# Kernel tuning notes

Hardware: AMD Instinct MI355X
Metric: run time of the kernel (lower is better)

## Reference

```python
import jax, jax.numpy as jnp
import numpy as np

B, K, D = 8, 4000, 256
H, DQ, DV = 8, 32, 32
WIN, PAD = 200, 50
STEP = WIN - 2 * PAD  # 100
BETA = 0.25


def setup_inputs() -> dict:
    key = jax.random.key(0)
    ks = jax.random.split(key, 14)
    s = 0.02
    return {
        "query": jax.random.normal(ks[0], (B, K, D), jnp.float32),
        "key": jax.random.normal(ks[1], (B, K, D), jnp.float32),
        "value": jax.random.normal(ks[2], (B, K, D), jnp.float32),
        "Wq": jax.random.normal(ks[3], (D, H * DQ), jnp.float32) * s,
        "bq": jax.random.normal(ks[4], (H * DQ,), jnp.float32) * s,
        "Wk": jax.random.normal(ks[5], (D, H * DQ), jnp.float32) * s,
        "bk": jax.random.normal(ks[6], (H * DQ,), jnp.float32) * s,
        "Wv": jax.random.normal(ks[7], (D, H * DV), jnp.float32) * s,
        "bv": jax.random.normal(ks[8], (H * DV,), jnp.float32) * s,
        "Wo": jax.random.normal(ks[9], (H * DV, D), jnp.float32) * s,
        "bo": jax.random.normal(ks[10], (D,), jnp.float32) * s,
    }


def _windows(x, n_win):
    starts = jnp.arange(n_win) * STEP
    idx = starts[:, None] + jnp.arange(WIN)[None, :]
    return x[:, :, idx, :]


def reference(query, key, value, Wq, bq, Wk, bk, Wv, bv, Wo, bo):
    b, k_len, d = query.shape
    pad = lambda t: jnp.pad(t, ((0, 0), (PAD, PAD), (0, 0)), mode='edge')  # replicate pad
    qp, kp, vp = pad(query), pad(key), pad(value)
    kpad = k_len + 2 * PAD
    n_win = (kpad - WIN) // STEP + 1

    def proj(x, Wm, bias, dh):
        y = x @ Wm + bias                       # [B, Kp, H*dh]
        return y.reshape(b, kpad, H, dh).transpose(0, 2, 1, 3)  # [B, H, Kp, dh]

    q = _windows(proj(qp, Wq, bq, DQ), n_win)
    kk = _windows(proj(kp, Wk, bk, DQ), n_win)
    v = _windows(proj(vp, Wv, bv, DV), n_win)

    scores = jnp.einsum('bhnid,bhnjd->bhnij', q, kk) / jnp.sqrt(jnp.float32(WIN))
    dist = jnp.abs(jnp.arange(WIN)[:, None] - jnp.arange(WIN)[None, :]).astype(scores.dtype)
    cauchy = (1.0 / (1.0 + BETA * dist * dist)) * (1.0 - jnp.eye(WIN, dtype=scores.dtype))
    scores = scores * cauchy
    causal = jnp.triu(jnp.ones((WIN, WIN), dtype=bool), k=1)  # attention_size is not None -> causal masking
    scores = jnp.where(causal, -jnp.inf, scores)
    attn = jax.nn.softmax(scores, axis=-1)
    out = jnp.einsum('bhnij,bhnjd->bhnid', attn, v)
    out = out[:, :, :, PAD:WIN - PAD, :].reshape(b, H, k_len, DV)
    out = out.transpose(0, 2, 1, 3).reshape(b, k_len, H * DV)  # heads concatenated, head-major slices
    return out @ Wo + bo
```

## Files before the change

kernel.cpp:

```cpp
#include <hip/hip_runtime.h>


typedef __bf16 bf16_t;
typedef __bf16 bf16x8 __attribute__((ext_vector_type(8)));
typedef float  f32x4  __attribute__((ext_vector_type(4)));

#define MFMA16(a, b, c) __builtin_amdgcn_mfma_f32_16x16x32_bf16((a), (b), (c), 0, 0, 0)

static __device__ __forceinline__ bf16x8 cvt8(float4 a, float4 b) {
  bf16x8 r;
  r[0] = (bf16_t)a.x; r[1] = (bf16_t)a.y; r[2] = (bf16_t)a.z; r[3] = (bf16_t)a.w;
  r[4] = (bf16_t)b.x; r[5] = (bf16_t)b.y; r[6] = (bf16_t)b.z; r[7] = (bf16_t)b.w;
  return r;
}

static __device__ __forceinline__ unsigned short bbits(bf16_t v) {
  union { bf16_t b; unsigned short u; } c; c.b = v; return c.u;
}

__global__ __launch_bounds__(256)
void prep_weights(const float* __restrict__ Wq, const float* __restrict__ Wk,
                  const float* __restrict__ Wv, const float* __restrict__ Wo,
                  bf16_t* __restrict__ wt) {
  const int mat  = blockIdx.x >> 6;
  const int tile = blockIdx.x & 63;
  const int kt = (tile >> 3) * 32, nt = (tile & 7) * 32;
  const float* W = (mat == 0) ? Wq : (mat == 1) ? Wk : (mat == 2) ? Wv : Wo;
  __shared__ float t[32][33];
  const int tx = threadIdx.x & 31, ty = threadIdx.x >> 5;
#pragma unroll
  for (int i = 0; i < 32; i += 8)
    t[ty + i][tx] = W[(size_t)(kt + ty + i) * 256 + nt + tx];
  __syncthreads();
  bf16_t* dst = wt + (size_t)mat * 65536;
#pragma unroll
  for (int i = 0; i < 32; i += 8)
    dst[(size_t)(nt + ty + i) * 256 + kt + tx] = (bf16_t)t[tx][ty + i];
}

template <int MODE>
__global__ __launch_bounds__(256)
void gemm256(const void* __restrict__ Xv, const bf16_t* __restrict__ Wt,
             const float* __restrict__ bias, void* __restrict__ Out, int M) {
  constexpr bool INB = (MODE == 3);
  const int m0 = blockIdx.x * 128;
  const int n0 = blockIdx.y * 128;
  __shared__ bf16_t la[128 * 40];
  __shared__ bf16_t lb[128 * 40];
  const int tid  = threadIdx.x;
  const int lane = tid & 63;
  const int wr   = ((tid >> 7) & 1) * 64;
  const int wc   = ((tid >> 6) & 1) * 64;
  const int lo   = lane & 15, hi = lane >> 4;
  const int arow = tid >> 1;
  const int acol = (tid & 1) * 16;
  int ar = m0 + arow; if (ar >= M) ar = M - 1;

  f32x4 acc[4][4] = {};

  for (int kk = 0; kk < 256; kk += 32) {
    if constexpr (!INB) {
      const float* X = (const float*)Xv + (size_t)ar * 256 + kk + acol;
      float4 x0 = ((const float4*)X)[0];
      float4 x1 = ((const float4*)X)[1];
      float4 x2 = ((const float4*)X)[2];
      float4 x3 = ((const float4*)X)[3];
      *(bf16x8*)&la[arow * 40 + acol]     = cvt8(x0, x1);
      *(bf16x8*)&la[arow * 40 + acol + 8] = cvt8(x2, x3);
    } else {
      const bf16_t* X = (const bf16_t*)Xv + (size_t)ar * 256 + kk + acol;
      *(bf16x8*)&la[arow * 40 + acol]     = ((const bf16x8*)X)[0];
      *(bf16x8*)&la[arow * 40 + acol + 8] = ((const bf16x8*)X)[1];
    }
    {
      const bf16_t* Wp = Wt + (size_t)(n0 + arow) * 256 + kk + acol;
      *(bf16x8*)&lb[arow * 40 + acol]     = ((const bf16x8*)Wp)[0];
      *(bf16x8*)&lb[arow * 40 + acol + 8] = ((const bf16x8*)Wp)[1];
    }
    __syncthreads();

    bf16x8 af[4], bfv[4];
#pragma unroll
    for (int mi = 0; mi < 4; ++mi)
      af[mi] = *(const bf16x8*)&la[(wr + mi * 16 + lo) * 40 + hi * 8];
#pragma unroll
    for (int ni = 0; ni < 4; ++ni)
      bfv[ni] = *(const bf16x8*)&lb[(wc + ni * 16 + lo) * 40 + hi * 8];
#pragma unroll
    for (int mi = 0; mi < 4; ++mi)
#pragma unroll
      for (int ni = 0; ni < 4; ++ni)
        acc[mi][ni] = MFMA16(af[mi], bfv[ni], acc[mi][ni]);
    __syncthreads();
  }

#pragma unroll
  for (int mi = 0; mi < 4; ++mi)
#pragma unroll
    for (int ni = 0; ni < 4; ++ni) {
      const int n   = n0 + wc + ni * 16 + lo;
      const float bia = bias[n];
      const int mb  = m0 + wr + mi * 16 + hi * 4;
      if (mb >= M) continue;
      if constexpr (MODE == 0) {
        bf16_t* O = (bf16_t*)Out;
#pragma unroll
        for (int r = 0; r < 4; ++r)
          O[(size_t)(mb + r) * 256 + n] = (bf16_t)(acc[mi][ni][r] + bia);
      } else if constexpr (MODE == 1) {
        const int b = mb / 4000, t = mb - b * 4000;
        bf16_t* O = (bf16_t*)Out;
#pragma unroll
        for (int r = 0; r < 4; ++r)
          O[((size_t)b * 4064 + t + 50 + r) * 256 + n] = (bf16_t)(acc[mi][ni][r] + bia);
      } else if constexpr (MODE == 2) {
        const int b = mb / 4000, t = mb - b * 4000;
        const int h = n >> 5, dv = n & 31;
        bf16_t* O = (bf16_t*)Out + ((size_t)((b * 8 + h) * 32 + dv)) * 4064 + t + 50;
        unsigned short e0 = bbits((bf16_t)(acc[mi][ni][0] + bia));
        unsigned short e1 = bbits((bf16_t)(acc[mi][ni][1] + bia));
        unsigned short e2 = bbits((bf16_t)(acc[mi][ni][2] + bia));
        unsigned short e3 = bbits((bf16_t)(acc[mi][ni][3] + bia));
        unsigned* O32 = (unsigned*)O;
        O32[0] = (unsigned)e0 | ((unsigned)e1 << 16);
        O32[1] = (unsigned)e2 | ((unsigned)e3 << 16);
      } else {
        float* O = (float*)Out;
#pragma unroll
        for (int r = 0; r < 4; ++r)
          O[(size_t)(mb + r) * 256 + n] = acc[mi][ni][r] + bia;
      }
    }
}

__global__ void fill_edges(bf16_t* __restrict__ kb, bf16_t* __restrict__ vt, int nb) {
  const int idx = blockIdx.x * 256 + threadIdx.x;
  const int kcnt = nb * 64 * 256;
  if (idx < kcnt) {
    const int b  = idx >> 14;
    const int pp = (idx >> 8) & 63;
    const int nn = idx & 255;
    const int p  = (pp < 50) ? pp : pp + 4000;
    bf16_t v = (pp < 50) ? kb[((size_t)b * 4064 + 50) * 256 + nn] : (bf16_t)0.f;
    kb[((size_t)b * 4064 + p) * 256 + nn] = v;
  } else {
    const int j  = idx - kcnt;
    const int bh = j >> 11;
    const int dv = (j >> 6) & 31;
    const int pp = j & 63;
    const int p  = (pp < 50) ? pp : pp + 4000;
    bf16_t v = (pp < 50) ? vt[((size_t)bh * 32 + dv) * 4064 + 50] : (bf16_t)0.f;
    vt[((size_t)bh * 32 + dv) * 4064 + p] = v;
  }
}

__global__ __launch_bounds__(448)
void attn_win(const bf16_t* __restrict__ qb, const bf16_t* __restrict__ kb,
              const bf16_t* __restrict__ vt, bf16_t* __restrict__ ao) {
  const int blk = blockIdx.x;
  const int n = blk % 40;
  const int h = (blk / 40) & 7;
  const int b = blk / 320;
  const int wv = threadIdx.x >> 6;
  const int lane = threadIdx.x & 63;
  const int lo = lane & 15, hi = lane >> 4;

  __shared__ __align__(16) bf16_t P[7][16][168];

  const int i0 = 50 + 16 * wv;
  int jtmax = (65 + 16 * wv) >> 4;
  if (jtmax > 9) jtmax = 9;

  int tq = n * 100 + 16 * wv + lo;
  if (tq > 3999) tq = 3999;
  const bf16x8 qf = *(const bf16x8*)&qb[((size_t)b * 4000 + tq) * 256 + h * 32 + hi * 8];

  const f32x4 zero = {0.f, 0.f, 0.f, 0.f};
  f32x4 sc[10];

#pragma unroll
  for (int jt = 0; jt < 10; ++jt) {
    if (jt <= jtmax) {
      const bf16x8 kf = *(const bf16x8*)&kb[((size_t)(b * 4064 + n * 100 + jt * 16 + lo)) * 256 + h * 32 + hi * 8];
      sc[jt] = MFMA16(qf, kf, zero);
    } else sc[jt] = zero;
  }

  const float scale = 0.07071067811865475f;
  const float NEG = -1e30f;
  float m4[4] = {0.f, 0.f, 0.f, 0.f};
#pragma unroll
  for (int jt = 0; jt < 10; ++jt) if (jt <= jtmax) {
#pragma unroll
    for (int r = 0; r < 4; ++r) {
      const int i = i0 + hi * 4 + r;
      const int j = jt * 16 + lo;
      const int d = i - j;
      float v;
      if (d < 0)        v = NEG;
      else if (d == 0)  v = 0.f;
      else {
        const float df = (float)d;
        v = sc[jt][r] * scale * __builtin_amdgcn_rcpf(1.f + 0.25f * df * df);
      }
      sc[jt][r] = v;
      m4[r] = fmaxf(m4[r], v);
    }
  }
#pragma unroll
  for (int msk = 1; msk < 16; msk <<= 1)
#pragma unroll
    for (int r = 0; r < 4; ++r)
      m4[r] = fmaxf(m4[r], __shfl_xor(m4[r], msk, 64));

  float s4[4] = {0.f, 0.f, 0.f, 0.f};
#pragma unroll
  for (int jt = 0; jt < 10; ++jt) if (jt <= jtmax) {
#pragma unroll
    for (int r = 0; r < 4; ++r) {
      const float e = __expf(sc[jt][r] - m4[r]);
      sc[jt][r] = e;
      s4[r] += e;
    }
  }
#pragma unroll
  for (int msk = 1; msk < 16; msk <<= 1)
#pragma unroll
    for (int r = 0; r < 4; ++r)
      s4[r] += __shfl_xor(s4[r], msk, 64);

  float ri4[4];
#pragma unroll
  for (int r = 0; r < 4; ++r) ri4[r] = 1.f / s4[r];

#pragma unroll
  for (int jt = 0; jt < 10; ++jt)
#pragma unroll
    for (int r = 0; r < 4; ++r)
      P[wv][hi * 4 + r][jt * 16 + lo] = (bf16_t)(sc[jt][r] * ri4[r]);

  f32x4 o0 = zero, o1 = zero;
  const size_t vbase = ((size_t)((b * 8 + h) * 32)) * 4064 + n * 100;
  const int reach = jtmax * 16 + 16;
#pragma unroll
  for (int kt = 0; kt < 5; ++kt) if (kt * 32 < reach) {
    const bf16x8 pf = *(const bf16x8*)&P[wv][lo][kt * 32 + hi * 8];
    const bf16x8 v0 = *(const bf16x8*)&vt[vbase + (size_t)lo * 4064 + kt * 32 + hi * 8];
    const bf16x8 v1 = *(const bf16x8*)&vt[vbase + (size_t)(16 + lo) * 4064 + kt * 32 + hi * 8];
    o0 = MFMA16(pf, v0, o0);
    o1 = MFMA16(pf, v1, o1);
  }

#pragma unroll
  for (int r = 0; r < 4; ++r) {
    const int i = i0 + hi * 4 + r;
    if (i < 150) {
      const int t = n * 100 + i - 50;
      bf16_t* op = &ao[((size_t)b * 4000 + t) * 256 + h * 32];
      op[lo]      = (bf16_t)o0[r];
      op[16 + lo] = (bf16_t)o1[r];
    }
  }
}

extern "C" void kernel_launch(void* const* d_in, const int* in_sizes, int n_in,
                              void* d_out, int out_size, void* d_ws, size_t ws_size,
                              hipStream_t stream) {
  (void)in_sizes; (void)n_in; (void)out_size;
  const float* query = (const float*)d_in[0];
  const float* key   = (const float*)d_in[1];
  const float* value = (const float*)d_in[2];
  const float* Wq = (const float*)d_in[3];
  const float* bq = (const float*)d_in[4];
  const float* Wk = (const float*)d_in[5];
  const float* bk = (const float*)d_in[6];
  const float* Wv = (const float*)d_in[7];
  const float* bv = (const float*)d_in[8];
  const float* Wo = (const float*)d_in[9];
  const float* bo = (const float*)d_in[10];

  int bc = 8;
  while (bc > 1 && 524288ull + (unsigned long long)bc * 8257536ull > (unsigned long long)ws_size)
    bc >>= 1;

  bf16_t* wt = (bf16_t*)d_ws;
  bf16_t* qb = wt + 4 * 65536;
  bf16_t* kb = qb + (size_t)bc * 4000 * 256;
  bf16_t* vt = kb + (size_t)bc * 4064 * 256;
  bf16_t* ao = vt + (size_t)bc * 8 * 32 * 4064;

  prep_weights<<<256, 256, 0, stream>>>(Wq, Wk, Wv, Wo, wt);

  for (int b0 = 0; b0 < 8; b0 += bc) {
    const int M = bc * 4000;
    const int mblk = (M + 127) / 128;
    const float* qx = query + (size_t)b0 * 4000 * 256;
    const float* kx = key   + (size_t)b0 * 4000 * 256;
    const float* vx = value + (size_t)b0 * 4000 * 256;
    float* ox = (float*)d_out + (size_t)b0 * 4000 * 256;

    gemm256<0><<<dim3(mblk, 2), 256, 0, stream>>>(qx, wt + 0 * 65536, bq, qb, M);
    gemm256<1><<<dim3(mblk, 2), 256, 0, stream>>>(kx, wt + 1 * 65536, bk, kb, M);
    gemm256<2><<<dim3(mblk, 2), 256, 0, stream>>>(vx, wt + 2 * 65536, bv, vt, M);
    fill_edges<<<bc * 128, 256, 0, stream>>>(kb, vt, bc);
    attn_win<<<bc * 320, 448, 0, stream>>>(qb, kb, vt, ao);
    gemm256<3><<<dim3(mblk, 2), 256, 0, stream>>>(ao, wt + 3 * 65536, bo, ox, M);
  }
}
```

Baseline: 116.8 us.

## Drop max-subtraction softmax, compute row sums via MFMA with ones, fold scale into Q

The attention kernel no longer does the two-pass softmax with max and sum shuffle reductions. It writes unnormalized exp(score·cauchy) values straight to LDS inside a rolled jt loop, gets the row sums from an extra MFMA against a ones vector, and normalizes the output at the end. The 1/sqrt(WIN) scale moves into the Q projection epilogue. This removes cross-lane reductions and cuts register pressure, but relies on scores being small enough that exp without max subtraction does not overflow, and the sums are built from bf16-rounded exponentials.

```diff
diff --git a/kernel.cpp b/kernel.cpp
--- a/kernel.cpp
+++ b/kernel.cpp
@@ -41,7 +41,8 @@
 template <int MODE>
 __global__ __launch_bounds__(256)
 void gemm256(const void* __restrict__ Xv, const bf16_t* __restrict__ Wt,
-             const float* __restrict__ bias, void* __restrict__ Out, int M) {
+             const float* __restrict__ bias, void* __restrict__ Out, int M,
+             float oscale) {
   constexpr bool INB = (MODE == 3);
   const int m0 = blockIdx.x * 128;
   const int n0 = blockIdx.y * 128;
@@ -106,7 +107,7 @@
         bf16_t* O = (bf16_t*)Out;
 #pragma unroll
         for (int r = 0; r < 4; ++r)
-          O[(size_t)(mb + r) * 256 + n] = (bf16_t)(acc[mi][ni][r] + bia);
+          O[(size_t)(mb + r) * 256 + n] = (bf16_t)((acc[mi][ni][r] + bia) * oscale);
       } else if constexpr (MODE == 1) {
         const int b = mb / 4000, t = mb - b * 4000;
         bf16_t* O = (bf16_t*)Out;
@@ -165,7 +166,7 @@
   const int lane = threadIdx.x & 63;
   const int lo = lane & 15, hi = lane >> 4;
 
-  __shared__ __align__(16) bf16_t P[7][16][168];
+  __shared__ __align__(16) bf16_t E[7][16][168];
 
   const int i0 = 50 + 16 * wv;
   int jtmax = (65 + 16 * wv) >> 4;
@@ -176,89 +177,54 @@
   const bf16x8 qf = *(const bf16x8*)&qb[((size_t)b * 4000 + tq) * 256 + h * 32 + hi * 8];
 
   const f32x4 zero = {0.f, 0.f, 0.f, 0.f};
-  f32x4 sc[10];
-
-#pragma unroll
-  for (int jt = 0; jt < 10; ++jt) {
-    if (jt <= jtmax) {
-      const bf16x8 kf = *(const bf16x8*)&kb[((size_t)(b * 4064 + n * 100 + jt * 16 + lo)) * 256 + h * 32 + hi * 8];
-      sc[jt] = MFMA16(qf, kf, zero);
-    } else sc[jt] = zero;
-  }
-
-  const float scale = 0.07071067811865475f;
-  const float NEG = -1e30f;
-  float m4[4] = {0.f, 0.f, 0.f, 0.f};
-#pragma unroll
-  for (int jt = 0; jt < 10; ++jt) if (jt <= jtmax) {
+
+  const int dbase = i0 + hi * 4 - lo;
+  for (int jt = 0; jt <= jtmax; ++jt) {
+    const bf16x8 kf = *(const bf16x8*)&kb[((size_t)(b * 4064 + n * 100 + jt * 16 + lo)) * 256 + h * 32 + hi * 8];
+    const f32x4 s = MFMA16(qf, kf, zero);
 #pragma unroll
     for (int r = 0; r < 4; ++r) {
-      const int i = i0 + hi * 4 + r;
-      const int j = jt * 16 + lo;
-      const int d = i - j;
-      float v;
-      if (d < 0)        v = NEG;
-      else if (d == 0)  v = 0.f;
-      else {
-        const float df = (float)d;
-        v = sc[jt][r] * scale * __builtin_amdgcn_rcpf(1.f + 0.25f * df * df);
-      }
-      sc[jt][r] = v;
-      m4[r] = fmaxf(m4[r], v);
-    }
-  }
-#pragma unroll
-  for (int msk = 1; msk < 16; msk <<= 1)
+      const int d = dbase + r - jt * 16;
+      const float df = (float)d;
+      float c = __builtin_amdgcn_rcpf(__builtin_fmaf(0.25f * df, df, 1.f));
+      c = (d == 0) ? 0.f : c;
+      float e = __expf(s[r] * c);
+      e = (d < 0) ? 0.f : e;
+      E[wv][hi * 4 + r][jt * 16 + lo] = (bf16_t)e;
+    }
+  }
+  for (int jt = jtmax + 1; jt < 10; ++jt) {
 #pragma unroll
     for (int r = 0; r < 4; ++r)
-      m4[r] = fmaxf(m4[r], __shfl_xor(m4[r], msk, 64));
-
-  float s4[4] = {0.f, 0.f, 0.f, 0.f};
-#pragma unroll
-  for (int jt = 0; jt < 10; ++jt) if (jt <= jtmax) {
-#pragma unroll
-    for (int r = 0; r < 4; ++r) {
-      const float e = __expf(sc[jt][r] - m4[r]);
-      sc[jt][r] = e;
-      s4[r] += e;
-    }
-  }
-#pragma unroll
-  for (int msk = 1; msk < 16; msk <<= 1)
-#pragma unroll
-    for (int r = 0; r < 4; ++r)
-      s4[r] += __shfl_xor(s4[r], msk, 64);
-
-  float ri4[4];
-#pragma unroll
-  for (int r = 0; r < 4; ++r) ri4[r] = 1.f / s4[r];
-
-#pragma unroll
-  for (int jt = 0; jt < 10; ++jt)
-#pragma unroll
-    for (int r = 0; r < 4; ++r)
-      P[wv][hi * 4 + r][jt * 16 + lo] = (bf16_t)(sc[jt][r] * ri4[r]);
-
-  f32x4 o0 = zero, o1 = zero;
+      E[wv][hi * 4 + r][jt * 16 + lo] = (bf16_t)0.f;
+  }
+
+  bf16x8 onesf;
+#pragma unroll
+  for (int u = 0; u < 8; ++u) onesf[u] = (bf16_t)1.0f;
+
+  f32x4 o0 = zero, o1 = zero, sm = zero;
   const size_t vbase = ((size_t)((b * 8 + h) * 32)) * 4064 + n * 100;
   const int reach = jtmax * 16 + 16;
 #pragma unroll
   for (int kt = 0; kt < 5; ++kt) if (kt * 32 < reach) {
-    const bf16x8 pf = *(const bf16x8*)&P[wv][lo][kt * 32 + hi * 8];
+    const bf16x8 pf = *(const bf16x8*)&E[wv][lo][kt * 32 + hi * 8];
     const bf16x8 v0 = *(const bf16x8*)&vt[vbase + (size_t)lo * 4064 + kt * 32 + hi * 8];
     const bf16x8 v1 = *(const bf16x8*)&vt[vbase + (size_t)(16 + lo) * 4064 + kt * 32 + hi * 8];
     o0 = MFMA16(pf, v0, o0);
     o1 = MFMA16(pf, v1, o1);
+    sm = MFMA16(pf, onesf, sm);
   }
 
 #pragma unroll
   for (int r = 0; r < 4; ++r) {
     const int i = i0 + hi * 4 + r;
     if (i < 150) {
+      const float ri = __builtin_amdgcn_rcpf(sm[r]);
       const int t = n * 100 + i - 50;
       bf16_t* op = &ao[((size_t)b * 4000 + t) * 256 + h * 32];
-      op[lo]      = (bf16_t)o0[r];
-      op[16 + lo] = (bf16_t)o1[r];
+      op[lo]      = (bf16_t)(o0[r] * ri);
+      op[16 + lo] = (bf16_t)(o1[r] * ri);
     }
   }
 }
@@ -291,6 +257,8 @@
 
   prep_weights<<<256, 256, 0, stream>>>(Wq, Wk, Wv, Wo, wt);
 
+  const float qscale = 0.07071067811865475f;
+
   for (int b0 = 0; b0 < 8; b0 += bc) {
     const int M = bc * 4000;
     const int mblk = (M + 127) / 128;
@@ -299,11 +267,11 @@
     const float* vx = value + (size_t)b0 * 4000 * 256;
     float* ox = (float*)d_out + (size_t)b0 * 4000 * 256;
 
-    gemm256<0><<<dim3(mblk, 2), 256, 0, stream>>>(qx, wt + 0 * 65536, bq, qb, M);
-    gemm256<1><<<dim3(mblk, 2), 256, 0, stream>>>(kx, wt + 1 * 65536, bk, kb, M);
-    gemm256<2><<<dim3(mblk, 2), 256, 0, stream>>>(vx, wt + 2 * 65536, bv, vt, M);
+    gemm256<0><<<dim3(mblk, 2), 256, 0, stream>>>(qx, wt + 0 * 65536, bq, qb, M, qscale);
+    gemm256<1><<<dim3(mblk, 2), 256, 0, stream>>>(kx, wt + 1 * 65536, bk, kb, M, 1.f);
+    gemm256<2><<<dim3(mblk, 2), 256, 0, stream>>>(vx, wt + 2 * 65536, bv, vt, M, 1.f);
     fill_edges<<<bc * 128, 256, 0, stream>>>(kb, vt, bc);
     attn_win<<<bc * 320, 448, 0, stream>>>(qb, kb, vt, ao);
-    gemm256<3><<<dim3(mblk, 2), 256, 0, stream>>>(ao, wt + 3 * 65536, bo, ox, M);
-  }
-}
+    gemm256<3><<<dim3(mblk, 2), 256, 0, stream>>>(ao, wt + 3 * 65536, bo, ox, M, 1.f);
+  }
+}
```

Result: faster. 112.5 us (-3.6%).
